# Kernel optimization log

Measured on AMD Instinct MI355X. Metric: run time of the kernel, lower is better.

The kernel has to match this reference:

```python
import jax, jax.numpy as jnp
import numpy as np

NEG_SLOPE = 0.2
EPS = 1e-16


def _segment_softmax(alpha, idx, num_segments):
    # alpha: [E, H], idx: [E] destination node ids
    m = jax.ops.segment_max(alpha, idx, num_segments=num_segments)
    alpha = jnp.exp(alpha - m[idx])
    s = jax.ops.segment_sum(alpha, idx, num_segments=num_segments)
    return alpha / (s[idx] + EPS)


def _gat_conv(x, src, dst, W, a_src, a_dst, b, concat):
    # x: [N, F_in], W: [F_in, H*C], a_src/a_dst: [H, C], b: [H*C] or [C]
    N = x.shape[0]
    H, C = a_src.shape
    h = (x @ W).reshape(N, H, C)                      # [N, H, C]
    alpha_s = jnp.einsum('nhc,hc->nh', h, a_src)      # [N, H]
    alpha_d = jnp.einsum('nhc,hc->nh', h, a_dst)      # [N, H]
    # PyG GATConv adds self-loops by default
    loop = jnp.arange(N, dtype=src.dtype)
    src2 = jnp.concatenate([src, loop])
    dst2 = jnp.concatenate([dst, loop])
    e = jax.nn.leaky_relu(alpha_s[src2] + alpha_d[dst2], NEG_SLOPE)  # [E+N, H]
    att = _segment_softmax(e, dst2, N)                # [E+N, H]
    msg = h[src2] * att[..., None]                    # [E+N, H, C]
    out = jax.ops.segment_sum(msg, dst2, num_segments=N)  # [N, H, C]
    out = out.reshape(N, H * C) if concat else out.mean(axis=1)
    return out + b


def setup_inputs() -> dict:
    key = jax.random.key(0)
    ks = jax.random.split(key, 16)
    N, E, F_in, H, C, C_out = 50000, 800000, 128, 4, 32, 64
    sc = lambda f: 1.0 / np.sqrt(f)
    inp = {
        'x': jax.random.normal(ks[0], (N, F_in), dtype=jnp.float32),
        'edge_index': jax.random.randint(ks[1], (2, E), 0, N, dtype=jnp.int64),
        'W0': jax.random.normal(ks[2], (F_in, H * C), dtype=jnp.float32) * sc(F_in),
        'a_src0': jax.random.normal(ks[3], (H, C), dtype=jnp.float32) * sc(C),
        'a_dst0': jax.random.normal(ks[4], (H, C), dtype=jnp.float32) * sc(C),
        'b0': jnp.zeros((H * C,), dtype=jnp.float32),
        'W1': jax.random.normal(ks[5], (H * C, H * C), dtype=jnp.float32) * sc(H * C),
        'a_src1': jax.random.normal(ks[6], (H, C), dtype=jnp.float32) * sc(C),
        'a_dst1': jax.random.normal(ks[7], (H, C), dtype=jnp.float32) * sc(C),
        'b1': jnp.zeros((H * C,), dtype=jnp.float32),
        'W2': jax.random.normal(ks[8], (H * C, H * C_out), dtype=jnp.float32) * sc(H * C),
        'a_src2': jax.random.normal(ks[9], (H, C_out), dtype=jnp.float32) * sc(C_out),
        'a_dst2': jax.random.normal(ks[10], (H, C_out), dtype=jnp.float32) * sc(C_out),
        'b2': jnp.zeros((C_out,), dtype=jnp.float32),
    }
    return inp


def reference(x, edge_index, W0, a_src0, a_dst0, b0, W1, a_src1, a_dst1, b1,
              W2, a_src2, a_dst2, b2):
    src, dst = edge_index[0], edge_index[1]
    # layer 0 (concat=True) -> relu (dropout is identity in eval mode)
    h = _gat_conv(x, src, dst, W0, a_src0, a_dst0, b0, concat=True)
    h = jax.nn.relu(h)
    # layer 1 (concat=True) -> relu
    h = _gat_conv(h, src, dst, W1, a_src1, a_dst1, b1, concat=True)
    h = jax.nn.relu(h)
    # layer 2 (concat=False, head mean)
    out = _gat_conv(h, src, dst, W2, a_src2, a_dst2, b2, concat=False)
    return out
```

## Files before the change

### kernel.cpp

```cpp
#include <hip/hip_runtime.h>
#include <hip/hip_fp16.h>
#include <math.h>

#define NEG_SLOPE 0.2f
#define GAT_EPS 1e-16f

typedef _Float16 f16x8 __attribute__((ext_vector_type(8)));
typedef float    f32x4 __attribute__((ext_vector_type(4)));

__device__ __forceinline__ float lrelu(float x) { return x > 0.f ? x : NEG_SLOPE * x; }

__device__ __forceinline__ void fma_row4(float4& a, float w, uint2 u) {
    const float2 f0 = __half22float2(*(const __half2*)&u.x);
    const float2 f1 = __half22float2(*(const __half2*)&u.y);
    a.x += w * f0.x; a.y += w * f0.y;
    a.z += w * f1.x; a.w += w * f1.y;
}

__device__ __forceinline__ void fma_row2(float2& a, float w, unsigned u) {
    const float2 f = __half22float2(*(const __half2*)&u);
    a.x += w * f.x; a.y += w * f.y;
}

__global__ __launch_bounds__(256) void gemm_tiled(
    const float* __restrict__ A, const float* __restrict__ B,
    float* __restrict__ C, __half* __restrict__ C16, int M, int K, int Ncol)
{
    __shared__ float As[16][65];
    __shared__ float Bs[16][64];

    const int t  = threadIdx.x;
    const int bm = blockIdx.x * 64;
    const int bn = blockIdx.y * 64;
    const int tx = t & 15;
    const int ty = t >> 4;

    float acc[4][4] = {};

    for (int k0 = 0; k0 < K; k0 += 16) {
        {
            const int r  = t >> 2;
            const int kq = (t & 3) * 4;
            float4 v = make_float4(0.f, 0.f, 0.f, 0.f);
            const int row = bm + r;
            if (row < M) v = *(const float4*)(A + (size_t)row * K + k0 + kq);
            As[kq + 0][r] = v.x; As[kq + 1][r] = v.y;
            As[kq + 2][r] = v.z; As[kq + 3][r] = v.w;
        }
        {
            const int k  = t >> 4;
            const int nq = (t & 15) * 4;
            float4 v = *(const float4*)(B + (size_t)(k0 + k) * Ncol + bn + nq);
            *(float4*)(&Bs[k][nq]) = v;
        }
        __syncthreads();

        #pragma unroll
        for (int k = 0; k < 16; ++k) {
            float a[4], b[4];
            #pragma unroll
            for (int i = 0; i < 4; ++i) a[i] = As[k][ty * 4 + i];
            #pragma unroll
            for (int j = 0; j < 4; ++j) b[j] = Bs[k][tx * 4 + j];
            #pragma unroll
            for (int i = 0; i < 4; ++i)
                #pragma unroll
                for (int j = 0; j < 4; ++j)
                    acc[i][j] += a[i] * b[j];
        }
        __syncthreads();
    }

    #pragma unroll
    for (int i = 0; i < 4; ++i) {
        const int row = bm + ty * 4 + i;
        if (row < M) {
            #pragma unroll
            for (int j = 0; j < 4; ++j) {
                const float v = acc[i][j];
                const size_t idx = (size_t)row * Ncol + bn + tx * 4 + j;
                if (C)   C[idx]   = v;
                if (C16) C16[idx] = __float2half_rn(v);
            }
        }
    }
}

__global__ __launch_bounds__(256) void pack_w2_kernel(
    const float* __restrict__ W2, __half* __restrict__ Wpk)
{
    const int idx = blockIdx.x * 256 + threadIdx.x;
    const int k = idx >> 8;
    const int c = idx & 255;
    const int ks = k >> 5;
    const int g  = (k >> 3) & 3;
    const int i  = k & 7;
    Wpk[((size_t)(ks * 256 + c) * 4 + g) * 8 + i] = __float2half_rn(W2[idx]);
}

__global__ __launch_bounds__(256) void gemm2_mfma(
    const __half* __restrict__ A16, const __half* __restrict__ Wpk,
    __half* __restrict__ C16, int M)
{
    const int t  = threadIdx.x;
    const int w  = t >> 6;
    const int l  = t & 63;
    const int bm = blockIdx.x * 64;
    const int bn = blockIdx.y * 64;
    const int row = bm + w * 16 + (l & 15);
    const int kg  = l >> 4;
    const bool rok = row < M;

    f32x4 acc[4] = {};

    #pragma unroll
    for (int ks = 0; ks < 4; ++ks) {
        f16x8 a = {};
        if (rok)
            a = *(const f16x8*)(A16 + (size_t)row * 128 + ks * 32 + kg * 8);
        #pragma unroll
        for (int f = 0; f < 4; ++f) {
            const f16x8 b = *(const f16x8*)(Wpk +
                ((size_t)(ks * 256 + bn + f * 16 + (l & 15)) * 4 + kg) * 8);
            acc[f] = __builtin_amdgcn_mfma_f32_16x16x32_f16(a, b, acc[f], 0, 0, 0);
        }
    }

    const int orow = bm + w * 16 + (l >> 4) * 4;
    #pragma unroll
    for (int f = 0; f < 4; ++f) {
        const int ccol = bn + f * 16 + (l & 15);
        #pragma unroll
        for (int r = 0; r < 4; ++r) {
            if (orow + r < M)
                C16[(size_t)(orow + r) * 256 + ccol] = __float2half_rn(acc[f][r]);
        }
    }
}

__global__ __launch_bounds__(256) void alpha_kernel(
    const float* __restrict__ h, const float* __restrict__ a_src,
    const float* __restrict__ a_dst, float* __restrict__ as_,
    float* __restrict__ ad_, int N, int HC, int C)
{
    const int i = blockIdx.x * blockDim.x + threadIdx.x;
    if (i >= N * 4) return;
    const int n  = i >> 2;
    const int hh = i & 3;
    const float* hp  = h + (size_t)n * HC + hh * C;
    const float* asp = a_src + hh * C;
    const float* adp = a_dst + hh * C;
    float s1 = 0.f, s2 = 0.f;
    for (int c = 0; c < C; c += 4) {
        const float4 v = *(const float4*)(hp + c);
        const float4 A = *(const float4*)(asp + c);
        const float4 D = *(const float4*)(adp + c);
        s1 += v.x * A.x + v.y * A.y + v.z * A.z + v.w * A.w;
        s2 += v.x * D.x + v.y * D.y + v.z * D.z + v.w * D.w;
    }
    as_[i] = s1;
    ad_[i] = s2;
}

__global__ __launch_bounds__(256) void alpha16_kernel(
    const __half* __restrict__ h, const float* __restrict__ a_src,
    const float* __restrict__ a_dst, float* __restrict__ as_,
    float* __restrict__ ad_, int N, int HC, int C)
{
    const int i = blockIdx.x * blockDim.x + threadIdx.x;
    if (i >= N * 4) return;
    const int n  = i >> 2;
    const int hh = i & 3;
    const __half* hp = h + (size_t)n * HC + hh * C;
    const float* asp = a_src + hh * C;
    const float* adp = a_dst + hh * C;
    float s1 = 0.f, s2 = 0.f;
    for (int c = 0; c < C; c += 2) {
        const float2 f = __half22float2(*(const __half2*)(hp + c));
        s1 += f.x * asp[c] + f.y * asp[c + 1];
        s2 += f.x * adp[c] + f.y * adp[c + 1];
    }
    as_[i] = s1;
    ad_[i] = s2;
}

__global__ __launch_bounds__(256) void zero_kernel(int* __restrict__ p, int n)
{
    const int i = blockIdx.x * 256 + threadIdx.x;
    if (i < n) p[i] = 0;
}

__global__ __launch_bounds__(256) void count_kernel(
    const int* __restrict__ ei, int* __restrict__ deg, int E)
{
    const int e = blockIdx.x * 256 + threadIdx.x;
    if (e < E) atomicAdd(&deg[ei[E + e]], 1);
}

__global__ __launch_bounds__(256) void scan_part_kernel(
    const int* __restrict__ deg, int* __restrict__ bsum, int N)
{
    __shared__ int red[256];
    const int b = blockIdx.x;
    const int t = threadIdx.x;
    const int base = b * 1024 + t * 4;
    int s = 0;
    #pragma unroll
    for (int i = 0; i < 4; ++i) {
        const int idx = base + i;
        if (idx < N) s += deg[idx];
    }
    red[t] = s;
    __syncthreads();
    for (int off = 128; off; off >>= 1) {
        if (t < off) red[t] += red[t + off];
        __syncthreads();
    }
    if (t == 0) bsum[b] = red[0];
}

__global__ __launch_bounds__(256) void scan_top_kernel(
    int* __restrict__ bsum, int B)
{
    __shared__ int sh[256];
    const int t = threadIdx.x;
    const int v = (t < B) ? bsum[t] : 0;
    sh[t] = v;
    __syncthreads();
    for (int off = 1; off < 256; off <<= 1) {
        const int u = (t >= off) ? sh[t - off] : 0;
        __syncthreads();
        sh[t] += u;
        __syncthreads();
    }
    if (t < B) bsum[t] = sh[t] - v;
}

__global__ __launch_bounds__(256) void scan_out_kernel(
    const int* __restrict__ deg, const int* __restrict__ bsum,
    int* __restrict__ rp, int N)
{
    __shared__ int red[256];
    const int b = blockIdx.x;
    const int t = threadIdx.x;
    const int base = b * 1024 + t * 4;
    int v[4]; int s = 0;
    #pragma unroll
    for (int i = 0; i < 4; ++i) {
        const int idx = base + i;
        v[i] = (idx < N) ? deg[idx] : 0;
        s += v[i];
    }
    red[t] = s;
    __syncthreads();
    for (int off = 1; off < 256; off <<= 1) {
        const int u = (t >= off) ? red[t - off] : 0;
        __syncthreads();
        red[t] += u;
        __syncthreads();
    }
    int run = bsum[b] + ((t > 0) ? red[t - 1] : 0);
    if (b == 0 && t == 0) rp[0] = 0;
    #pragma unroll
    for (int i = 0; i < 4; ++i) {
        const int idx = base + i;
        if (idx < N) { rp[idx + 1] = run; run += v[i]; }
    }
}

__global__ __launch_bounds__(256) void scatter_kernel(
    const int* __restrict__ ei, int* __restrict__ rp, int* __restrict__ col, int E)
{
    const int e = blockIdx.x * 256 + threadIdx.x;
    if (e < E) {
        const int dn  = ei[E + e];
        const int pos = atomicAdd(&rp[dn + 1], 1);
        col[pos] = ei[e];
    }
}

__global__ __launch_bounds__(256) void agg32_kernel(
    const __half* __restrict__ h16, const float* __restrict__ as_,
    const float* __restrict__ ad_, const int* __restrict__ rp,
    const int* __restrict__ col, const float* __restrict__ bias,
    float* __restrict__ out, __half* __restrict__ out16, int N)
{
    const int n = blockIdx.x * 4 + (threadIdx.x >> 6);
    if (n >= N) return;
    const int lane = threadIdx.x & 63;
    const int head = lane >> 4;
    const int start = rp[n];
    const int d     = rp[n + 1] - start;
    const float adn = ad_[n * 4 + head];

    float ss = 0.f;
    float2 a0 = {0.f, 0.f}, a1 = {0.f, 0.f}, a2 = {0.f, 0.f}, a3 = {0.f, 0.f};

    int e = 0;
    for (; e + 4 <= d; e += 4) {
        const int s0 = col[start + e + 0];
        const int s1 = col[start + e + 1];
        const int s2 = col[start + e + 2];
        const int s3 = col[start + e + 3];
        const float w0 = __expf(lrelu(as_[s0 * 4 + head] + adn));
        const float w1 = __expf(lrelu(as_[s1 * 4 + head] + adn));
        const float w2 = __expf(lrelu(as_[s2 * 4 + head] + adn));
        const float w3 = __expf(lrelu(as_[s3 * 4 + head] + adn));
        const unsigned u0 = *(const unsigned*)(h16 + (size_t)s0 * 128 + 2 * lane);
        const unsigned u1 = *(const unsigned*)(h16 + (size_t)s1 * 128 + 2 * lane);
        const unsigned u2 = *(const unsigned*)(h16 + (size_t)s2 * 128 + 2 * lane);
        const unsigned u3 = *(const unsigned*)(h16 + (size_t)s3 * 128 + 2 * lane);
        ss += (w0 + w1) + (w2 + w3);
        fma_row2(a0, w0, u0);
        fma_row2(a1, w1, u1);
        fma_row2(a2, w2, u2);
        fma_row2(a3, w3, u3);
    }
    for (; e < d; ++e) {
        const int s = col[start + e];
        const float wt = __expf(lrelu(as_[s * 4 + head] + adn));
        const unsigned u = *(const unsigned*)(h16 + (size_t)s * 128 + 2 * lane);
        ss += wt;
        fma_row2(a0, wt, u);
    }
    {
        const float wt = __expf(lrelu(as_[n * 4 + head] + adn));
        const unsigned u = *(const unsigned*)(h16 + (size_t)n * 128 + 2 * lane);
        ss += wt;
        fma_row2(a0, wt, u);
    }

    float2 v;
    v.x = (a0.x + a1.x) + (a2.x + a3.x);
    v.y = (a0.y + a1.y) + (a2.y + a3.y);
    const float inv = 1.f / (ss + GAT_EPS);
    const float2 bb = *(const float2*)(bias + 2 * lane);
    v.x = fmaxf(v.x * inv + bb.x, 0.f);
    v.y = fmaxf(v.y * inv + bb.y, 0.f);
    *(float2*)(out + (size_t)n * 128 + 2 * lane) = v;
    if (out16)
        *(__half2*)(out16 + (size_t)n * 128 + 2 * lane) = __floats2half2_rn(v.x, v.y);
}

__global__ __launch_bounds__(256) void agg64_mean_kernel(
    const __half* __restrict__ h16, const float* __restrict__ as_,
    const float* __restrict__ ad_, const int* __restrict__ rp,
    const int* __restrict__ col, const float* __restrict__ b2,
    float* __restrict__ out, int N)
{
    const int n = blockIdx.x * 4 + (threadIdx.x >> 6);
    if (n >= N) return;
    const int lane = threadIdx.x & 63;
    const int head = lane >> 4;
    const int start = rp[n];
    const int d     = rp[n + 1] - start;
    const float adn = ad_[n * 4 + head];

    float ss = 0.f;
    float4 a0 = {0,0,0,0}, a1 = {0,0,0,0}, a2 = {0,0,0,0}, a3 = {0,0,0,0};

    int e = 0;
    for (; e + 4 <= d; e += 4) {
        const int s0 = col[start + e + 0];
        const int s1 = col[start + e + 1];
        const int s2 = col[start + e + 2];
        const int s3 = col[start + e + 3];
        const float w0 = __expf(lrelu(as_[s0 * 4 + head] + adn));
        const float w1 = __expf(lrelu(as_[s1 * 4 + head] + adn));
        const float w2 = __expf(lrelu(as_[s2 * 4 + head] + adn));
        const float w3 = __expf(lrelu(as_[s3 * 4 + head] + adn));
        const uint2 u0 = *(const uint2*)(h16 + (size_t)s0 * 256 + 4 * lane);
        const uint2 u1 = *(const uint2*)(h16 + (size_t)s1 * 256 + 4 * lane);
        const uint2 u2 = *(const uint2*)(h16 + (size_t)s2 * 256 + 4 * lane);
        const uint2 u3 = *(const uint2*)(h16 + (size_t)s3 * 256 + 4 * lane);
        ss += (w0 + w1) + (w2 + w3);
        fma_row4(a0, w0, u0);
        fma_row4(a1, w1, u1);
        fma_row4(a2, w2, u2);
        fma_row4(a3, w3, u3);
    }
    for (; e < d; ++e) {
        const int s = col[start + e];
        const float wt = __expf(lrelu(as_[s * 4 + head] + adn));
        const uint2 u = *(const uint2*)(h16 + (size_t)s * 256 + 4 * lane);
        ss += wt;
        fma_row4(a0, wt, u);
    }
    {
        const float wt = __expf(lrelu(as_[n * 4 + head] + adn));
        const uint2 u = *(const uint2*)(h16 + (size_t)n * 256 + 4 * lane);
        ss += wt;
        fma_row4(a0, wt, u);
    }

    const float inv = 1.f / (ss + GAT_EPS);
    float vx = ((a0.x + a1.x) + (a2.x + a3.x)) * inv;
    float vy = ((a0.y + a1.y) + (a2.y + a3.y)) * inv;
    float vz = ((a0.z + a1.z) + (a2.z + a3.z)) * inv;
    float vw = ((a0.w + a1.w) + (a2.w + a3.w)) * inv;

    vx += __shfl_xor(vx, 16); vx += __shfl_xor(vx, 32);
    vy += __shfl_xor(vy, 16); vy += __shfl_xor(vy, 32);
    vz += __shfl_xor(vz, 16); vz += __shfl_xor(vz, 32);
    vw += __shfl_xor(vw, 16); vw += __shfl_xor(vw, 32);

    if (lane < 16) {
        const float4 bb = *(const float4*)(b2 + 4 * lane);
        float4 o;
        o.x = 0.25f * vx + bb.x;
        o.y = 0.25f * vy + bb.y;
        o.z = 0.25f * vz + bb.z;
        o.w = 0.25f * vw + bb.w;
        *(float4*)(out + (size_t)n * 64 + 4 * lane) = o;
    }
}

extern "C" void kernel_launch(void* const* d_in, const int* in_sizes, int n_in,
                              void* d_out, int out_size, void* d_ws, size_t ws_size,
                              hipStream_t stream)
{
    const float* x   = (const float*)d_in[0];
    const int*   ei  = (const int*)d_in[1];
    const float* W0  = (const float*)d_in[2];
    const float* aS0 = (const float*)d_in[3];
    const float* aD0 = (const float*)d_in[4];
    const float* b0  = (const float*)d_in[5];
    const float* W1  = (const float*)d_in[6];
    const float* aS1 = (const float*)d_in[7];
    const float* aD1 = (const float*)d_in[8];
    const float* b1  = (const float*)d_in[9];
    const float* W2  = (const float*)d_in[10];
    const float* aS2 = (const float*)d_in[11];
    const float* aD2 = (const float*)d_in[12];
    const float* b2  = (const float*)d_in[13];

    const int N = in_sizes[0] / 128;
    const int E = in_sizes[1] / 2;

    float* ws     = (float*)d_ws;
    float* bufA   = ws;
    __half* h16a  = (__half*)(ws + (size_t)N * 128);
    __half* o16   = (__half*)(ws + (size_t)N * 192);
    __half* h2_16 = (__half*)ws;
    float* o_buf  = ws + (size_t)N * 256;
    float* as_buf = ws + (size_t)N * 384;
    float* ad_buf = ws + (size_t)N * 388;
    int*   rp     = (int*)(ws + (size_t)N * 392);
    int*   col    = (int*)(ws + (size_t)N * 394);
    int*   deg    = (int*)(ws + (size_t)N * 394) + E;
    int*   bsum   = deg + N;
    __half* Wpk   = (__half*)(bsum + 256);

    const int TB  = 256;
    const int gN  = (N + TB - 1) / TB;
    const int gE  = (E + TB - 1) / TB;
    const int gNH = (N * 4 + TB - 1) / TB;
    const int gS  = (N + 1023) / 1024;
    const int gA  = (N + 3) / 4;

    zero_kernel<<<gN, TB, 0, stream>>>(deg, N);
    count_kernel<<<gE, TB, 0, stream>>>(ei, deg, E);
    pack_w2_kernel<<<128, TB, 0, stream>>>(W2, Wpk);
    scan_part_kernel<<<gS, TB, 0, stream>>>(deg, bsum, N);
    scan_top_kernel<<<1, TB, 0, stream>>>(bsum, gS);
    scan_out_kernel<<<gS, TB, 0, stream>>>(deg, bsum, rp, N);
    scatter_kernel<<<gE, TB, 0, stream>>>(ei, rp, col, E);

    {
        dim3 g((N + 63) / 64, 2);
        gemm_tiled<<<g, TB, 0, stream>>>(x, W0, bufA, h16a, N, 128, 128);
        alpha_kernel<<<gNH, TB, 0, stream>>>(bufA, aS0, aD0, as_buf, ad_buf, N, 128, 32);
        agg32_kernel<<<gA, TB, 0, stream>>>(h16a, as_buf, ad_buf, rp, col, b0, o_buf, nullptr, N);
    }
    {
        dim3 g((N + 63) / 64, 2);
        gemm_tiled<<<g, TB, 0, stream>>>(o_buf, W1, bufA, h16a, N, 128, 128);
        alpha_kernel<<<gNH, TB, 0, stream>>>(bufA, aS1, aD1, as_buf, ad_buf, N, 128, 32);
        agg32_kernel<<<gA, TB, 0, stream>>>(h16a, as_buf, ad_buf, rp, col, b1, o_buf, o16, N);
    }
    {
        dim3 g((N + 63) / 64, 4);
        gemm2_mfma<<<g, TB, 0, stream>>>(o16, Wpk, h2_16, N);
        alpha16_kernel<<<gNH, TB, 0, stream>>>(h2_16, aS2, aD2, as_buf, ad_buf, N, 256, 64);
        agg64_mean_kernel<<<gA, TB, 0, stream>>>(h2_16, as_buf, ad_buf, rp, col, b2, (float*)d_out, N);
    }
}
```

Baseline: 517.6 us.

## Use fp16 MFMA GEMM for all three layers and drop fp32 intermediates

Replaces the fp32 shared-memory tiled GEMM of layers 0 and 1 with the generalized fp16 MFMA GEMM already used for layer 2. Input x is cast to fp16 once, and all three weight matrices are packed into the MFMA layout. The attention logits are now computed from fp16 features, and the aggregation kernels write only fp16 outputs, removing the fp32 feature buffers and their memory traffic. This lowers precision for the layer-0 and layer-1 GEMMs and logits and adds a cast kernel plus extra pack launches.

```diff
diff --git a/kernel.cpp b/kernel.cpp
--- a/kernel.cpp
+++ b/kernel.cpp
@@ -22,85 +22,31 @@
     a.x += w * f.x; a.y += w * f.y;
 }
 
-__global__ __launch_bounds__(256) void gemm_tiled(
-    const float* __restrict__ A, const float* __restrict__ B,
-    float* __restrict__ C, __half* __restrict__ C16, int M, int K, int Ncol)
-{
-    __shared__ float As[16][65];
-    __shared__ float Bs[16][64];
-
-    const int t  = threadIdx.x;
-    const int bm = blockIdx.x * 64;
-    const int bn = blockIdx.y * 64;
-    const int tx = t & 15;
-    const int ty = t >> 4;
-
-    float acc[4][4] = {};
-
-    for (int k0 = 0; k0 < K; k0 += 16) {
-        {
-            const int r  = t >> 2;
-            const int kq = (t & 3) * 4;
-            float4 v = make_float4(0.f, 0.f, 0.f, 0.f);
-            const int row = bm + r;
-            if (row < M) v = *(const float4*)(A + (size_t)row * K + k0 + kq);
-            As[kq + 0][r] = v.x; As[kq + 1][r] = v.y;
-            As[kq + 2][r] = v.z; As[kq + 3][r] = v.w;
-        }
-        {
-            const int k  = t >> 4;
-            const int nq = (t & 15) * 4;
-            float4 v = *(const float4*)(B + (size_t)(k0 + k) * Ncol + bn + nq);
-            *(float4*)(&Bs[k][nq]) = v;
-        }
-        __syncthreads();
-
-        #pragma unroll
-        for (int k = 0; k < 16; ++k) {
-            float a[4], b[4];
-            #pragma unroll
-            for (int i = 0; i < 4; ++i) a[i] = As[k][ty * 4 + i];
-            #pragma unroll
-            for (int j = 0; j < 4; ++j) b[j] = Bs[k][tx * 4 + j];
-            #pragma unroll
-            for (int i = 0; i < 4; ++i)
-                #pragma unroll
-                for (int j = 0; j < 4; ++j)
-                    acc[i][j] += a[i] * b[j];
-        }
-        __syncthreads();
-    }
-
-    #pragma unroll
-    for (int i = 0; i < 4; ++i) {
-        const int row = bm + ty * 4 + i;
-        if (row < M) {
-            #pragma unroll
-            for (int j = 0; j < 4; ++j) {
-                const float v = acc[i][j];
-                const size_t idx = (size_t)row * Ncol + bn + tx * 4 + j;
-                if (C)   C[idx]   = v;
-                if (C16) C16[idx] = __float2half_rn(v);
-            }
-        }
-    }
-}
-
-__global__ __launch_bounds__(256) void pack_w2_kernel(
-    const float* __restrict__ W2, __half* __restrict__ Wpk)
+__global__ __launch_bounds__(256) void cast16_kernel(
+    const float* __restrict__ src, __half* __restrict__ dst, int n2)
+{
+    const int i = blockIdx.x * 256 + threadIdx.x;
+    if (i < n2) {
+        const float2 v = *(const float2*)(src + 2 * i);
+        *(__half2*)(dst + 2 * i) = __floats2half2_rn(v.x, v.y);
+    }
+}
+
+__global__ __launch_bounds__(256) void pack_w_kernel(
+    const float* __restrict__ W, __half* __restrict__ Wpk, int Ncol)
 {
     const int idx = blockIdx.x * 256 + threadIdx.x;
-    const int k = idx >> 8;
-    const int c = idx & 255;
+    const int k = idx / Ncol;
+    const int c = idx - k * Ncol;
     const int ks = k >> 5;
     const int g  = (k >> 3) & 3;
     const int i  = k & 7;
-    Wpk[((size_t)(ks * 256 + c) * 4 + g) * 8 + i] = __float2half_rn(W2[idx]);
-}
-
-__global__ __launch_bounds__(256) void gemm2_mfma(
+    Wpk[((size_t)(ks * Ncol + c) * 4 + g) * 8 + i] = __float2half_rn(W[idx]);
+}
+
+__global__ __launch_bounds__(256) void gemm_mfma(
     const __half* __restrict__ A16, const __half* __restrict__ Wpk,
-    __half* __restrict__ C16, int M)
+    __half* __restrict__ C16, int M, int Ncol)
 {
     const int t  = threadIdx.x;
     const int w  = t >> 6;
@@ -121,7 +67,7 @@
         #pragma unroll
         for (int f = 0; f < 4; ++f) {
             const f16x8 b = *(const f16x8*)(Wpk +
-                ((size_t)(ks * 256 + bn + f * 16 + (l & 15)) * 4 + kg) * 8);
+                ((size_t)(ks * Ncol + bn + f * 16 + (l & 15)) * 4 + kg) * 8);
             acc[f] = __builtin_amdgcn_mfma_f32_16x16x32_f16(a, b, acc[f], 0, 0, 0);
         }
     }
@@ -133,33 +79,9 @@
         #pragma unroll
         for (int r = 0; r < 4; ++r) {
             if (orow + r < M)
-                C16[(size_t)(orow + r) * 256 + ccol] = __float2half_rn(acc[f][r]);
+                C16[(size_t)(orow + r) * Ncol + ccol] = __float2half_rn(acc[f][r]);
         }
     }
-}
-
-__global__ __launch_bounds__(256) void alpha_kernel(
-    const float* __restrict__ h, const float* __restrict__ a_src,
-    const float* __restrict__ a_dst, float* __restrict__ as_,
-    float* __restrict__ ad_, int N, int HC, int C)
-{
-    const int i = blockIdx.x * blockDim.x + threadIdx.x;
-    if (i >= N * 4) return;
-    const int n  = i >> 2;
-    const int hh = i & 3;
-    const float* hp  = h + (size_t)n * HC + hh * C;
-    const float* asp = a_src + hh * C;
-    const float* adp = a_dst + hh * C;
-    float s1 = 0.f, s2 = 0.f;
-    for (int c = 0; c < C; c += 4) {
-        const float4 v = *(const float4*)(hp + c);
-        const float4 A = *(const float4*)(asp + c);
-        const float4 D = *(const float4*)(adp + c);
-        s1 += v.x * A.x + v.y * A.y + v.z * A.z + v.w * A.w;
-        s2 += v.x * D.x + v.y * D.y + v.z * D.z + v.w * D.w;
-    }
-    as_[i] = s1;
-    ad_[i] = s2;
 }
 
 __global__ __launch_bounds__(256) void alpha16_kernel(
@@ -283,7 +205,7 @@
     const __half* __restrict__ h16, const float* __restrict__ as_,
     const float* __restrict__ ad_, const int* __restrict__ rp,
     const int* __restrict__ col, const float* __restrict__ bias,
-    float* __restrict__ out, __half* __restrict__ out16, int N)
+    __half* __restrict__ out16, int N)
 {
     const int n = blockIdx.x * 4 + (threadIdx.x >> 6);
     if (n >= N) return;
@@ -337,9 +259,7 @@
     const float2 bb = *(const float2*)(bias + 2 * lane);
     v.x = fmaxf(v.x * inv + bb.x, 0.f);
     v.y = fmaxf(v.y * inv + bb.y, 0.f);
-    *(float2*)(out + (size_t)n * 128 + 2 * lane) = v;
-    if (out16)
-        *(__half2*)(out16 + (size_t)n * 128 + 2 * lane) = __floats2half2_rn(v.x, v.y);
+    *(__half2*)(out16 + (size_t)n * 128 + 2 * lane) = __floats2half2_rn(v.x, v.y);
 }
 
 __global__ __launch_bounds__(256) void agg64_mean_kernel(
@@ -438,18 +358,18 @@
     const int E = in_sizes[1] / 2;
 
     float* ws     = (float*)d_ws;
-    float* bufA   = ws;
-    __half* h16a  = (__half*)(ws + (size_t)N * 128);
-    __half* o16   = (__half*)(ws + (size_t)N * 192);
     __half* h2_16 = (__half*)ws;
-    float* o_buf  = ws + (size_t)N * 256;
-    float* as_buf = ws + (size_t)N * 384;
-    float* ad_buf = ws + (size_t)N * 388;
-    int*   rp     = (int*)(ws + (size_t)N * 392);
-    int*   col    = (int*)(ws + (size_t)N * 394);
-    int*   deg    = (int*)(ws + (size_t)N * 394) + E;
+    __half* h16   = (__half*)(ws + (size_t)N * 128);
+    __half* a16   = (__half*)(ws + (size_t)N * 192);
+    float* as_buf = ws + (size_t)N * 256;
+    float* ad_buf = ws + (size_t)N * 260;
+    int*   rp     = (int*)(ws + (size_t)N * 264);
+    int*   col    = (int*)(ws + (size_t)N * 266);
+    int*   deg    = (int*)(ws + (size_t)N * 266) + E;
     int*   bsum   = deg + N;
-    __half* Wpk   = (__half*)(bsum + 256);
+    __half* Wpk0  = (__half*)(bsum + 256);
+    __half* Wpk1  = Wpk0 + 16384;
+    __half* Wpk2  = Wpk1 + 16384;
 
     const int TB  = 256;
     const int gN  = (N + TB - 1) / TB;
@@ -460,7 +380,10 @@
 
     zero_kernel<<<gN, TB, 0, stream>>>(deg, N);
     count_kernel<<<gE, TB, 0, stream>>>(ei, deg, E);
-    pack_w2_kernel<<<128, TB, 0, stream>>>(W2, Wpk);
+    pack_w_kernel<<<64, TB, 0, stream>>>(W0, Wpk0, 128);
+    pack_w_kernel<<<64, TB, 0, stream>>>(W1, Wpk1, 128);
+    pack_w_kernel<<<128, TB, 0, stream>>>(W2, Wpk2, 256);
+    cast16_kernel<<<(N * 64 + TB - 1) / TB, TB, 0, stream>>>(x, a16, N * 64);
     scan_part_kernel<<<gS, TB, 0, stream>>>(deg, bsum, N);
     scan_top_kernel<<<1, TB, 0, stream>>>(bsum, gS);
     scan_out_kernel<<<gS, TB, 0, stream>>>(deg, bsum, rp, N);
@@ -468,19 +391,19 @@
 
     {
         dim3 g((N + 63) / 64, 2);
-        gemm_tiled<<<g, TB, 0, stream>>>(x, W0, bufA, h16a, N, 128, 128);
-        alpha_kernel<<<gNH, TB, 0, stream>>>(bufA, aS0, aD0, as_buf, ad_buf, N, 128, 32);
-        agg32_kernel<<<gA, TB, 0, stream>>>(h16a, as_buf, ad_buf, rp, col, b0, o_buf, nullptr, N);
+        gemm_mfma<<<g, TB, 0, stream>>>(a16, Wpk0, h16, N, 128);
+        alpha16_kernel<<<gNH, TB, 0, stream>>>(h16, aS0, aD0, as_buf, ad_buf, N, 128, 32);
+        agg32_kernel<<<gA, TB, 0, stream>>>(h16, as_buf, ad_buf, rp, col, b0, a16, N);
     }
     {
         dim3 g((N + 63) / 64, 2);
-        gemm_tiled<<<g, TB, 0, stream>>>(o_buf, W1, bufA, h16a, N, 128, 128);
-        alpha_kernel<<<gNH, TB, 0, stream>>>(bufA, aS1, aD1, as_buf, ad_buf, N, 128, 32);
-        agg32_kernel<<<gA, TB, 0, stream>>>(h16a, as_buf, ad_buf, rp, col, b1, o_buf, o16, N);
+        gemm_mfma<<<g, TB, 0, stream>>>(a16, Wpk1, h16, N, 128);
+        alpha16_kernel<<<gNH, TB, 0, stream>>>(h16, aS1, aD1, as_buf, ad_buf, N, 128, 32);
+        agg32_kernel<<<gA, TB, 0, stream>>>(h16, as_buf, ad_buf, rp, col, b1, a16, N);
     }
     {
         dim3 g((N + 63) / 64, 4);
-        gemm2_mfma<<<g, TB, 0, stream>>>(o16, Wpk, h2_16, N);
+        gemm_mfma<<<g, TB, 0, stream>>>(a16, Wpk2, h2_16, N, 256);
         alpha16_kernel<<<gNH, TB, 0, stream>>>(h2_16, aS2, aD2, as_buf, ad_buf, N, 256, 64);
         agg64_mean_kernel<<<gA, TB, 0, stream>>>(h2_16, as_buf, ad_buf, rp, col, b2, (float*)d_out, N);
     }
```

New measurement: 505.7 us. 1.02x faster.
